# Optimization experiments

Measured on AMD Instinct MI355X. Metric: run time of the kernel, lower is better.

## Reference

```python
import jax, jax.numpy as jnp
import numpy as np

N = 100000   # nodes
E = 1600000  # edges
IN = 128     # in_channels
H = 96       # hidden
G = 512      # graphs in batch


def setup_inputs() -> dict:
    key = jax.random.key(0)
    ks = jax.random.split(key, 11)
    x = jax.random.normal(ks[0], (N, IN), jnp.float32)
    edge_index = jax.random.randint(ks[1], (2, E), 0, N)
    batch = jnp.sort(jax.random.randint(ks[2], (N,), 0, G))
    def lin(k, fan_in, fan_out):
        lim = 1.0 / np.sqrt(fan_in)
        kw, kb = jax.random.split(k)
        W = jax.random.uniform(kw, (fan_in, fan_out), jnp.float32, -lim, lim)
        b = jax.random.uniform(kb, (fan_out,), jnp.float32, -lim, lim)
        return W, b
    W1, b1 = lin(ks[3], IN, H)
    W2, b2 = lin(ks[4], H, H)
    Wn, bn = lin(ks[5], 2 * H, 1)
    Wg, bg = lin(ks[6], 4 * H, 1)
    return dict(x=x, edge_index=edge_index, batch=batch,
                W1=W1, b1=b1, W2=W2, b2=b2, Wn=Wn, bn=bn, Wg=Wg, bg=bg)


def reference(x, edge_index, batch, W1, b1, W2, b2, Wn, bn, Wg, bg):
    # --- GCN normalization with self-loops: D^-1/2 (A+I) D^-1/2 ---
    loops = jnp.arange(N)
    src = jnp.concatenate([edge_index[0], loops])  # [E+N]
    dst = jnp.concatenate([edge_index[1], loops])
    deg = jax.ops.segment_sum(jnp.ones_like(dst, jnp.float32), dst, num_segments=N)
    dis = jnp.where(deg > 0, jax.lax.rsqrt(jnp.maximum(deg, 1.0)), 0.0)
    norm = dis[src] * dis[dst]  # [E+N]

    def gcn_conv(h, W, b):
        hw = h @ W                                # transform first (smaller msgs)
        msg = hw[src] * norm[:, None]             # gather + scale  [E+N, H]
        return jax.ops.segment_sum(msg, dst, num_segments=N) + b

    h1 = jax.nn.relu(gcn_conv(x, W1, b1))         # dropout: eval no-op
    h2 = jax.nn.relu(gcn_conv(h1, W2, b2))
    h = jnp.concatenate([h1, h2], axis=1)         # [N, 2H]

    node_logits = (h @ Wn + bn).reshape(-1)       # [N]

    cnt = jax.ops.segment_sum(jnp.ones((N,), jnp.float32), batch, num_segments=G)
    meanp = jax.ops.segment_sum(h, batch, num_segments=G) / jnp.maximum(cnt, 1.0)[:, None]
    maxp = jax.ops.segment_max(h, batch, num_segments=G)
    maxp = jnp.where(cnt[:, None] > 0, maxp, 0.0)
    pooled = jnp.concatenate([meanp, maxp], axis=1)  # [G, 4H]

    graph_logits = (pooled @ Wg + bg).reshape(-1)    # [G]
    return graph_logits, node_logits
```

## Files before the change

### kernel.cpp

```cpp
#include <hip/hip_runtime.h>
#include <hip/hip_fp16.h>

#define NN 100000
#define NE 1600000
#define INC 128
#define HID 96
#define NG 512

#define GEMM1_BLOCKS 1563
#define G2_BLOCKS 1563

#define BK_SHIFT 9
#define BK_SIZE 512
#define NBK 196
#define A_EPB 16384
#define A_BLOCKS 98

typedef _Float16 half8 __attribute__((ext_vector_type(8)));
typedef float f32x4 __attribute__((ext_vector_type(4)));

__global__ __launch_bounds__(256) void k_pack_a1(const int* __restrict__ dst,
                                                 int* __restrict__ histAB,
                                                 const float* __restrict__ W2,
                                                 __half* __restrict__ W2frag) {
    const int tid = threadIdx.x;
    if (blockIdx.x < A_BLOCKS) {
        __shared__ int cnt[NBK];
        int ab = blockIdx.x;
        for (int i = tid; i < NBK; i += 256) cnt[i] = 0;
        __syncthreads();
        int e0 = ab * A_EPB;
#pragma unroll 4
        for (int q = 0; q < A_EPB / 256; ++q) {
            int e = e0 + q * 256 + tid;
            if (e < NE) atomicAdd(&cnt[dst[e] >> BK_SHIFT], 1);
        }
        __syncthreads();
        for (int i = tid; i < NBK; i += 256) histAB[ab * NBK + i] = cnt[i];
        return;
    }
    int p = (blockIdx.x - A_BLOCKS) * 256 + tid;
    if (p >= 3 * 6 * 64) return;
    int kc = p / 384;
    int rem = p - kc * 384;
    int ct = rem >> 6;
    int l = rem & 63;
#pragma unroll
    for (int i = 0; i < 8; ++i) {
        int k = kc * 32 + ((l >> 4) << 3) + i;
        int c = ct * 16 + (l & 15);
        W2frag[p * 8 + i] = __float2half(W2[k * HID + c]);
    }
}

__global__ __launch_bounds__(256) void k_scanS(int* __restrict__ histAB, int* __restrict__ boff) {
    __shared__ int tot[256];
    int t = threadIdx.x;
    int run = 0;
    if (t < NBK) {
        for (int blk = 0; blk < A_BLOCKS; ++blk) {
            int idx = blk * NBK + t;
            int v = histAB[idx];
            histAB[idx] = run;
            run += v;
        }
    }
    tot[t] = (t < NBK) ? run : 0;
    __syncthreads();
    for (int ofs = 1; ofs < 256; ofs <<= 1) {
        int v = (t >= ofs) ? tot[t - ofs] : 0;
        __syncthreads();
        tot[t] += v;
        __syncthreads();
    }
    if (t == 0) boff[0] = 0;
    if (t < NBK) boff[t + 1] = tot[t];
}

__global__ __launch_bounds__(256) void k_gemm1_a3(
        const float* __restrict__ X, const float* __restrict__ W, __half* __restrict__ Yh,
        const int* __restrict__ src, const int* __restrict__ dst,
        const int* __restrict__ boff, const int* __restrict__ histAB,
        unsigned* __restrict__ tmp) {
    __shared__ float xsT[32][64];
    __shared__ float ws[32 * 96];
    const int tid = threadIdx.x;

    if (blockIdx.x < A_BLOCKS) {
        int* base = (int*)&xsT[0][0];
        int* lcnt = base + NBK;
        int ab = blockIdx.x;
        for (int i = tid; i < NBK; i += 256) {
            base[i] = boff[i] + histAB[ab * NBK + i];
            lcnt[i] = 0;
        }
        __syncthreads();
        int e0 = ab * A_EPB;
#pragma unroll 4
        for (int q = 0; q < A_EPB / 256; ++q) {
            int e = e0 + q * 256 + tid;
            if (e < NE) {
                int d = dst[e];
                int bk = d >> BK_SHIFT;
                int lp = atomicAdd(&lcnt[bk], 1);
                tmp[base[bk] + lp] = (unsigned)src[e] | ((unsigned)(d & (BK_SIZE - 1)) << 17);
            }
        }
        return;
    }

    const int row0 = (blockIdx.x - A_BLOCKS) * 64;
    const int rg = tid >> 4;
    const int cg = tid & 15;
    const int r0 = rg * 4, c0 = cg * 6;
    float acc[4][6] = {};
    const int srow = tid & 63;
    const int sq = tid >> 6;

    for (int k0 = 0; k0 < INC; k0 += 32) {
        {
            int grow = row0 + srow;
            float4 v = make_float4(0.f, 0.f, 0.f, 0.f);
            float4 u = make_float4(0.f, 0.f, 0.f, 0.f);
            if (grow < NN) {
                v = *(const float4*)&X[(size_t)grow * INC + k0 + sq * 4];
                u = *(const float4*)&X[(size_t)grow * INC + k0 + (sq + 4) * 4];
            }
            xsT[sq * 4 + 0][srow] = v.x;
            xsT[sq * 4 + 1][srow] = v.y;
            xsT[sq * 4 + 2][srow] = v.z;
            xsT[sq * 4 + 3][srow] = v.w;
            xsT[(sq + 4) * 4 + 0][srow] = u.x;
            xsT[(sq + 4) * 4 + 1][srow] = u.y;
            xsT[(sq + 4) * 4 + 2][srow] = u.z;
            xsT[(sq + 4) * 4 + 3][srow] = u.w;
        }
        {
            const float4* wsrc = (const float4*)(W + k0 * 96);
            float4* wdst = (float4*)ws;
            wdst[tid] = wsrc[tid];
            wdst[tid + 256] = wsrc[tid + 256];
            wdst[tid + 512] = wsrc[tid + 512];
        }
        __syncthreads();
#pragma unroll
        for (int kk = 0; kk < 32; ++kk) {
            float4 xv = *(const float4*)&xsT[kk][r0];
            float wv[6];
            *(float2*)&wv[0] = *(const float2*)&ws[kk * 96 + c0];
            *(float2*)&wv[2] = *(const float2*)&ws[kk * 96 + c0 + 2];
            *(float2*)&wv[4] = *(const float2*)&ws[kk * 96 + c0 + 4];
            float xr[4] = {xv.x, xv.y, xv.z, xv.w};
#pragma unroll
            for (int i = 0; i < 4; ++i)
#pragma unroll
                for (int j = 0; j < 6; ++j) acc[i][j] += xr[i] * wv[j];
        }
        __syncthreads();
    }
#pragma unroll
    for (int i = 0; i < 4; ++i) {
        int grow = row0 + r0 + i;
        if (grow >= NN) break;
        __half2* yp = (__half2*)&Yh[(size_t)grow * HID + c0];
        yp[0] = __floats2half2_rn(acc[i][0], acc[i][1]);
        yp[1] = __floats2half2_rn(acc[i][2], acc[i][3]);
        yp[2] = __floats2half2_rn(acc[i][4], acc[i][5]);
    }
}

__global__ __launch_bounds__(256) void k_B1(const unsigned* __restrict__ tmp,
                                            const int* __restrict__ boff,
                                            int* __restrict__ off, float* __restrict__ dis) {
    __shared__ int cnt[BK_SIZE];
    __shared__ int psum[256];
    const int t = threadIdx.x;
    const int b = blockIdx.x;
    const int nb = b << BK_SHIFT;
    const int rbeg = boff[b], rend = boff[b + 1];
    cnt[t] = 0; cnt[t + 256] = 0;
    __syncthreads();
    for (int e = rbeg + t; e < rend; e += 256) {
        unsigned u = tmp[e];
        atomicAdd(&cnt[u >> 17], 1);
    }
    __syncthreads();
    int c0 = cnt[2 * t], c1 = cnt[2 * t + 1];
    int pairSum = c0 + c1;
    psum[t] = pairSum;
    __syncthreads();
    for (int ofs = 1; ofs < 256; ofs <<= 1) {
        int v = (t >= ofs) ? psum[t - ofs] : 0;
        __syncthreads();
        psum[t] += v;
        __syncthreads();
    }
    int pairExcl = psum[t] - pairSum;
    int node0 = nb + 2 * t, node1 = node0 + 1;
    if (node0 < NN) {
        off[node0] = rbeg + pairExcl;
        dis[node0] = rsqrtf((float)(c0 + 1));
    }
    if (node1 < NN) {
        off[node1] = rbeg + pairExcl + c0;
        dis[node1] = rsqrtf((float)(c1 + 1));
    }
    if (b == NBK - 1 && t == 0) off[NN] = rend;
}

__global__ __launch_bounds__(256) void k_B2(const unsigned* __restrict__ tmp,
                                            const int* __restrict__ boff,
                                            const int* __restrict__ off,
                                            const float* __restrict__ dis,
                                            int2* __restrict__ ssrcw) {
    __shared__ int cnt[BK_SIZE];
    const int tid = threadIdx.x;
    const int b = blockIdx.x;
    const int nb = b << BK_SHIFT;
    const int rbeg = boff[b], rend = boff[b + 1];
    cnt[tid] = 0; cnt[tid + 256] = 0;
    __syncthreads();
    for (int e = rbeg + tid; e < rend; e += 256) {
        unsigned u = tmp[e];
        int s = (int)(u & 0x1FFFFu);
        int dl = (int)(u >> 17);
        int d = nb + dl;
        int pos = off[d] + atomicAdd(&cnt[dl], 1);
        float w = dis[s] * dis[d];
        ssrcw[pos] = make_int2(s, __float_as_int(w));
    }
}

__global__ __launch_bounds__(256) void k_gemm2(const __half* __restrict__ Xh,
                                               const __half* __restrict__ W2frag,
                                               __half* __restrict__ Yh) {
    __shared__ __half w2s[9216];
    const int tid = threadIdx.x;
    {
        half8* d8 = (half8*)w2s;
        const half8* s8 = (const half8*)W2frag;
        for (int i = tid; i < 1152; i += 256) d8[i] = s8[i];
    }
    __syncthreads();
    const int w = tid >> 6;
    const int l = tid & 63;
    const int row0 = blockIdx.x * 64 + w * 16;
    int arow = row0 + (l & 15);
    if (arow >= NN) arow = NN - 1;
    f32x4 acc[6] = {};
#pragma unroll
    for (int kc = 0; kc < 3; ++kc) {
        half8 a = *(const half8*)&Xh[(size_t)arow * HID + kc * 32 + ((l >> 4) << 3)];
#pragma unroll
        for (int ct = 0; ct < 6; ++ct) {
            half8 b = *(const half8*)&w2s[((kc * 6 + ct) * 64 + l) * 8];
            acc[ct] = __builtin_amdgcn_mfma_f32_16x16x32_f16(a, b, acc[ct], 0, 0, 0);
        }
    }
    const int orow = row0 + ((l >> 4) << 2);
    const int col = l & 15;
#pragma unroll
    for (int ct = 0; ct < 6; ++ct)
#pragma unroll
        for (int i = 0; i < 4; ++i) {
            int r = orow + i;
            if (r < NN) Yh[(size_t)r * HID + ct * 16 + col] = __float2half(acc[ct][i]);
        }
}

template <int PHASE>
__global__ __launch_bounds__(256) void k_agg(const __half* __restrict__ Ah,
                                             const int2* __restrict__ ssrcw,
                                             const int* __restrict__ off,
                                             const float* __restrict__ dis,
                                             const float* __restrict__ bias,
                                             const float* __restrict__ Wn,
                                             const float* __restrict__ bn,
                                             __half* __restrict__ outh,
                                             float* __restrict__ nodeOut) {
    int gid = blockIdx.x * blockDim.x + threadIdx.x;
    int d = gid >> 4;
    int t = gid & 15;
    if (d >= NN) return;
    const int beg = off[d], end = off[d + 1];
    const float dd = dis[d];
    const __half2* ad2 = (const __half2*)(Ah + (size_t)d * HID);
    float2 s0 = __half22float2(ad2[t]);
    float2 s1 = __half22float2(ad2[t + 16]);
    float2 s2 = __half22float2(ad2[t + 32]);
    const float dd2 = dd * dd;
    float a0x = s0.x * dd2, a0y = s0.y * dd2;
    float a1x = s1.x * dd2, a1y = s1.y * dd2;
    float a2x = s2.x * dd2, a2y = s2.y * dd2;
    int j = beg;
    for (; j + 7 < end; j += 8) {
        int2 e[8];
#pragma unroll
        for (int q = 0; q < 8; ++q) e[q] = ssrcw[j + q];
        float w[8];
        const __half2* ap[8];
#pragma unroll
        for (int q = 0; q < 8; ++q) {
            w[q] = __int_as_float(e[q].y);
            ap[q] = (const __half2*)(Ah + (size_t)e[q].x * HID);
        }
        __half2 g0[8], g1[8], g2[8];
#pragma unroll
        for (int q = 0; q < 8; ++q) {
            g0[q] = ap[q][t];
            g1[q] = ap[q][t + 16];
            g2[q] = ap[q][t + 32];
        }
#pragma unroll
        for (int q = 0; q < 8; ++q) {
            float2 f0 = __half22float2(g0[q]);
            float2 f1 = __half22float2(g1[q]);
            float2 f2 = __half22float2(g2[q]);
            a0x += f0.x * w[q]; a0y += f0.y * w[q];
            a1x += f1.x * w[q]; a1y += f1.y * w[q];
            a2x += f2.x * w[q]; a2y += f2.y * w[q];
        }
    }
    for (; j < end; ++j) {
        int2 e0 = ssrcw[j];
        float w0 = __int_as_float(e0.y);
        const __half2* a0 = (const __half2*)(Ah + (size_t)e0.x * HID);
        float2 f0 = __half22float2(a0[t]);
        float2 f1 = __half22float2(a0[t + 16]);
        float2 f2 = __half22float2(a0[t + 32]);
        a0x += f0.x * w0; a0y += f0.y * w0;
        a1x += f1.x * w0; a1y += f1.y * w0;
        a2x += f2.x * w0; a2y += f2.y * w0;
    }
    const float2* b2p = (const float2*)bias;
    float2 b0 = b2p[t], b1 = b2p[t + 16], b2 = b2p[t + 32];
    float h0x = fmaxf(a0x + b0.x, 0.f), h0y = fmaxf(a0y + b0.y, 0.f);
    float h1x = fmaxf(a1x + b1.x, 0.f), h1y = fmaxf(a1y + b1.y, 0.f);
    float h2x = fmaxf(a2x + b2.x, 0.f), h2y = fmaxf(a2y + b2.y, 0.f);
    __half2* o2 = (__half2*)(outh + (size_t)d * HID);
    o2[t]      = __floats2half2_rn(h0x, h0y);
    o2[t + 16] = __floats2half2_rn(h1x, h1y);
    o2[t + 32] = __floats2half2_rn(h2x, h2y);

    const int woff = (PHASE == 1) ? 0 : 96;
    const float2* wn2 = (const float2*)(Wn + woff);
    float2 w0v = wn2[t], w1v = wn2[t + 16], w2v = wn2[t + 32];
    float partial = h0x * w0v.x + h0y * w0v.y + h1x * w1v.x + h1y * w1v.y +
                    h2x * w2v.x + h2y * w2v.y;
#pragma unroll
    for (int m = 8; m; m >>= 1) partial += __shfl_down(partial, m, 16);
    if (t == 0) {
        if (PHASE == 1) nodeOut[d] = partial + bn[0];
        else            nodeOut[d] += partial;
    }
}

__global__ __launch_bounds__(768) void k_pool(const __half* __restrict__ h1,
                                              const __half* __restrict__ h2,
                                              const int* __restrict__ batch,
                                              const float* __restrict__ Wg,
                                              const float* __restrict__ bg,
                                              float* __restrict__ out) {
    int g = blockIdx.x;
    int tid = threadIdx.x;
    int way = tid / 192;
    int f = tid - way * 192;

    int lo = 0, hi = NN;
    while (lo < hi) { int mid = (lo + hi) >> 1; if (batch[mid] < g) lo = mid + 1; else hi = mid; }
    int start = lo;
    hi = NN;
    while (lo < hi) { int mid = (lo + hi) >> 1; if (batch[mid] < g + 1) lo = mid + 1; else hi = mid; }
    int end = lo;

    const __half* hsrc = (f < HID) ? h1 : h2;
    int ff = (f < HID) ? f : f - HID;
    float sum = 0.f, mx = 0.f;
    for (int n = start + way; n < end; n += 4) {
        float v = __half2float(hsrc[(size_t)n * HID + ff]);
        sum += v;
        mx = fmaxf(mx, v);
    }
    __shared__ float rsum[4][192];
    __shared__ float rmax[4][192];
    rsum[way][f] = sum;
    rmax[way][f] = mx;
    __syncthreads();
    if (way == 0) {
        sum = rsum[0][f] + rsum[1][f] + rsum[2][f] + rsum[3][f];
        mx = fmaxf(fmaxf(rmax[0][f], rmax[1][f]), fmaxf(rmax[2][f], rmax[3][f]));
        float cnt = (float)(end - start);
        float mean = sum / fmaxf(cnt, 1.0f);
        rsum[0][f] = mean * Wg[f] + mx * Wg[192 + f];
    }
    __syncthreads();
    if (tid < 64) {
        float acc = rsum[0][tid] + rsum[0][tid + 64] + rsum[0][tid + 128];
#pragma unroll
        for (int m = 32; m; m >>= 1) acc += __shfl_down(acc, m, 64);
        if (tid == 0) out[g] = acc + bg[0];
    }
}

extern "C" void kernel_launch(void* const* d_in, const int* in_sizes, int n_in,
                              void* d_out, int out_size, void* d_ws, size_t ws_size,
                              hipStream_t stream) {
    const float* x    = (const float*)d_in[0];
    const int*   ei   = (const int*)d_in[1];
    const int*   srcp = ei;
    const int*   dstp = ei + NE;
    const int*   batch = (const int*)d_in[2];
    const float* W1 = (const float*)d_in[3];
    const float* b1 = (const float*)d_in[4];
    const float* W2 = (const float*)d_in[5];
    const float* b2 = (const float*)d_in[6];
    const float* Wn = (const float*)d_in[7];
    const float* bn = (const float*)d_in[8];
    const float* Wg = (const float*)d_in[9];
    const float* bg = (const float*)d_in[10];
    float* out = (float*)d_out;

    char* p = (char*)d_ws;
    auto alloc = [&](size_t bytes) {
        char* r = p;
        p += (bytes + 255) & ~(size_t)255;
        return (void*)r;
    };
    float*    dis    = (float*)alloc(NN * 4);
    int*      off    = (int*)alloc((NN + 1) * 4);
    int*      boff   = (int*)alloc((NBK + 1) * 4);
    int*      histAB = (int*)alloc((size_t)A_BLOCKS * NBK * 4);
    unsigned* tmp    = (unsigned*)alloc((size_t)NE * 4);
    int2*     ssrcw  = (int2*)alloc((size_t)NE * 8);
    __half*   Ah     = (__half*)alloc((size_t)NN * HID * 2);
    __half*   H1h    = (__half*)alloc((size_t)NN * HID * 2);
    __half*   H2h    = (__half*)alloc((size_t)NN * HID * 2);
    __half*   W2frag = (__half*)alloc(9216 * 2);

    const int TPB = 256;

    k_pack_a1<<<A_BLOCKS + 5, TPB, 0, stream>>>(dstp, histAB, W2, W2frag);
    k_scanS<<<1, 256, 0, stream>>>(histAB, boff);
    k_gemm1_a3<<<A_BLOCKS + GEMM1_BLOCKS, 256, 0, stream>>>(
        x, W1, Ah, srcp, dstp, boff, histAB, tmp);
    k_B1<<<NBK, 256, 0, stream>>>(tmp, boff, off, dis);
    k_B2<<<NBK, 256, 0, stream>>>(tmp, boff, off, dis, ssrcw);

    const int aggThreads = NN * 16;
    float* nodeOut = out + NG;

    k_agg<1><<<(aggThreads + TPB - 1) / TPB, TPB, 0, stream>>>(Ah, ssrcw, off, dis, b1, Wn, bn, H1h, nodeOut);

    k_gemm2<<<G2_BLOCKS, 256, 0, stream>>>(H1h, W2frag, Ah);

    k_agg<2><<<(aggThreads + TPB - 1) / TPB, TPB, 0, stream>>>(Ah, ssrcw, off, dis, b2, Wn, bn, H2h, nodeOut);

    k_pool<<<NG, 768, 0, stream>>>(H1h, H2h, batch, Wg, bg, out);
}
```

Baseline: 261.7 us.

## Use fp16 MFMA for the first GEMM with prepacked W1 fragments

Replaces the fp32 register-tiled FMA GEMM (X@W1) with an MFMA 16x16x32 fp16 path. W1 is prepacked into MFMA B-fragment layout by the existing pack kernel and staged in LDS, and X rows are loaded straight from global memory and converted to fp16 in registers. This removes the LDS transpose staging and the scalar FMA work, at the cost of fp16 rounding of inputs and scattered 2-byte output stores.

```diff
diff --git a/kernel.cpp b/kernel.cpp
--- a/kernel.cpp
+++ b/kernel.cpp
@@ -21,7 +21,9 @@
 
 __global__ __launch_bounds__(256) void k_pack_a1(const int* __restrict__ dst,
                                                  int* __restrict__ histAB,
+                                                 const float* __restrict__ W1,
                                                  const float* __restrict__ W2,
+                                                 __half* __restrict__ W1frag,
                                                  __half* __restrict__ W2frag) {
     const int tid = threadIdx.x;
     if (blockIdx.x < A_BLOCKS) {
@@ -40,16 +42,30 @@
         return;
     }
     int p = (blockIdx.x - A_BLOCKS) * 256 + tid;
-    if (p >= 3 * 6 * 64) return;
-    int kc = p / 384;
-    int rem = p - kc * 384;
-    int ct = rem >> 6;
-    int l = rem & 63;
-#pragma unroll
-    for (int i = 0; i < 8; ++i) {
-        int k = kc * 32 + ((l >> 4) << 3) + i;
-        int c = ct * 16 + (l & 15);
-        W2frag[p * 8 + i] = __float2half(W2[k * HID + c]);
+    if (p < 1536) {
+        int kc = p / 384;
+        int rem = p - kc * 384;
+        int ct = rem >> 6;
+        int l = rem & 63;
+#pragma unroll
+        for (int i = 0; i < 8; ++i) {
+            int k = kc * 32 + ((l >> 4) << 3) + i;
+            int c = ct * 16 + (l & 15);
+            W1frag[p * 8 + i] = __float2half(W1[k * HID + c]);
+        }
+    } else {
+        int q = p - 1536;
+        if (q >= 1152) return;
+        int kc = q / 384;
+        int rem = q - kc * 384;
+        int ct = rem >> 6;
+        int l = rem & 63;
+#pragma unroll
+        for (int i = 0; i < 8; ++i) {
+            int k = kc * 32 + ((l >> 4) << 3) + i;
+            int c = ct * 16 + (l & 15);
+            W2frag[q * 8 + i] = __float2half(W2[k * HID + c]);
+        }
     }
 }
 
@@ -78,16 +94,16 @@
 }
 
 __global__ __launch_bounds__(256) void k_gemm1_a3(
-        const float* __restrict__ X, const float* __restrict__ W, __half* __restrict__ Yh,
+        const float* __restrict__ X, const __half* __restrict__ W1frag,
+        __half* __restrict__ Yh,
         const int* __restrict__ src, const int* __restrict__ dst,
         const int* __restrict__ boff, const int* __restrict__ histAB,
         unsigned* __restrict__ tmp) {
-    __shared__ float xsT[32][64];
-    __shared__ float ws[32 * 96];
+    __shared__ __half w1s[12288];
     const int tid = threadIdx.x;
 
     if (blockIdx.x < A_BLOCKS) {
-        int* base = (int*)&xsT[0][0];
+        int* base = (int*)w1s;
         int* lcnt = base + NBK;
         int ab = blockIdx.x;
         for (int i = tid; i < NBK; i += 256) {
@@ -109,64 +125,43 @@
         return;
     }
 
-    const int row0 = (blockIdx.x - A_BLOCKS) * 64;
-    const int rg = tid >> 4;
-    const int cg = tid & 15;
-    const int r0 = rg * 4, c0 = cg * 6;
-    float acc[4][6] = {};
-    const int srow = tid & 63;
-    const int sq = tid >> 6;
-
-    for (int k0 = 0; k0 < INC; k0 += 32) {
-        {
-            int grow = row0 + srow;
-            float4 v = make_float4(0.f, 0.f, 0.f, 0.f);
-            float4 u = make_float4(0.f, 0.f, 0.f, 0.f);
-            if (grow < NN) {
-                v = *(const float4*)&X[(size_t)grow * INC + k0 + sq * 4];
-                u = *(const float4*)&X[(size_t)grow * INC + k0 + (sq + 4) * 4];
-            }
-            xsT[sq * 4 + 0][srow] = v.x;
-            xsT[sq * 4 + 1][srow] = v.y;
-            xsT[sq * 4 + 2][srow] = v.z;
-            xsT[sq * 4 + 3][srow] = v.w;
-            xsT[(sq + 4) * 4 + 0][srow] = u.x;
-            xsT[(sq + 4) * 4 + 1][srow] = u.y;
-            xsT[(sq + 4) * 4 + 2][srow] = u.z;
-            xsT[(sq + 4) * 4 + 3][srow] = u.w;
-        }
-        {
-            const float4* wsrc = (const float4*)(W + k0 * 96);
-            float4* wdst = (float4*)ws;
-            wdst[tid] = wsrc[tid];
-            wdst[tid + 256] = wsrc[tid + 256];
-            wdst[tid + 512] = wsrc[tid + 512];
-        }
-        __syncthreads();
-#pragma unroll
-        for (int kk = 0; kk < 32; ++kk) {
-            float4 xv = *(const float4*)&xsT[kk][r0];
-            float wv[6];
-            *(float2*)&wv[0] = *(const float2*)&ws[kk * 96 + c0];
-            *(float2*)&wv[2] = *(const float2*)&ws[kk * 96 + c0 + 2];
-            *(float2*)&wv[4] = *(const float2*)&ws[kk * 96 + c0 + 4];
-            float xr[4] = {xv.x, xv.y, xv.z, xv.w};
-#pragma unroll
-            for (int i = 0; i < 4; ++i)
-#pragma unroll
-                for (int j = 0; j < 6; ++j) acc[i][j] += xr[i] * wv[j];
-        }
-        __syncthreads();
-    }
-#pragma unroll
-    for (int i = 0; i < 4; ++i) {
-        int grow = row0 + r0 + i;
-        if (grow >= NN) break;
-        __half2* yp = (__half2*)&Yh[(size_t)grow * HID + c0];
-        yp[0] = __floats2half2_rn(acc[i][0], acc[i][1]);
-        yp[1] = __floats2half2_rn(acc[i][2], acc[i][3]);
-        yp[2] = __floats2half2_rn(acc[i][4], acc[i][5]);
-    }
+    {
+        half8* d8 = (half8*)w1s;
+        const half8* s8 = (const half8*)W1frag;
+        for (int i = tid; i < 1536; i += 256) d8[i] = s8[i];
+    }
+    __syncthreads();
+    const int w = tid >> 6;
+    const int l = tid & 63;
+    const int row0 = (blockIdx.x - A_BLOCKS) * 64 + w * 16;
+    int arow = row0 + (l & 15);
+    if (arow >= NN) arow = NN - 1;
+    f32x4 acc[6] = {};
+#pragma unroll
+    for (int kc = 0; kc < 4; ++kc) {
+        const float* xp = &X[(size_t)arow * INC + kc * 32 + ((l >> 4) << 3)];
+        float4 xa = *(const float4*)xp;
+        float4 xb = *(const float4*)(xp + 4);
+        half8 a;
+        a[0] = (_Float16)xa.x; a[1] = (_Float16)xa.y;
+        a[2] = (_Float16)xa.z; a[3] = (_Float16)xa.w;
+        a[4] = (_Float16)xb.x; a[5] = (_Float16)xb.y;
+        a[6] = (_Float16)xb.z; a[7] = (_Float16)xb.w;
+#pragma unroll
+        for (int ct = 0; ct < 6; ++ct) {
+            half8 b = *(const half8*)&w1s[((kc * 6 + ct) * 64 + l) * 8];
+            acc[ct] = __builtin_amdgcn_mfma_f32_16x16x32_f16(a, b, acc[ct], 0, 0, 0);
+        }
+    }
+    const int orow = row0 + ((l >> 4) << 2);
+    const int col = l & 15;
+#pragma unroll
+    for (int ct = 0; ct < 6; ++ct)
+#pragma unroll
+        for (int i = 0; i < 4; ++i) {
+            int r = orow + i;
+            if (r < NN) Yh[(size_t)r * HID + ct * 16 + col] = __float2half(acc[ct][i]);
+        }
 }
 
 __global__ __launch_bounds__(256) void k_B1(const unsigned* __restrict__ tmp,
@@ -435,14 +430,15 @@
     __half*   Ah     = (__half*)alloc((size_t)NN * HID * 2);
     __half*   H1h    = (__half*)alloc((size_t)NN * HID * 2);
     __half*   H2h    = (__half*)alloc((size_t)NN * HID * 2);
+    __half*   W1frag = (__half*)alloc(12288 * 2);
     __half*   W2frag = (__half*)alloc(9216 * 2);
 
     const int TPB = 256;
 
-    k_pack_a1<<<A_BLOCKS + 5, TPB, 0, stream>>>(dstp, histAB, W2, W2frag);
+    k_pack_a1<<<A_BLOCKS + 11, TPB, 0, stream>>>(dstp, histAB, W1, W2, W1frag, W2frag);
     k_scanS<<<1, 256, 0, stream>>>(histAB, boff);
     k_gemm1_a3<<<A_BLOCKS + GEMM1_BLOCKS, 256, 0, stream>>>(
-        x, W1, Ah, srcp, dstp, boff, histAB, tmp);
+        x, W1frag, Ah, srcp, dstp, boff, histAB, tmp);
     k_B1<<<NBK, 256, 0, stream>>>(tmp, boff, off, dis);
     k_B2<<<NBK, 256, 0, stream>>>(tmp, boff, off, dis, ssrcw);
 
```

Result: no change. 259.5 us (-0.8%).
